# Kernel tuning notes

Hardware: AMD Instinct MI355X
Metric: run time of the kernel (lower is better)

The kernel has to match this reference:

```python
import jax, jax.numpy as jnp
import numpy as np

DIM = 1024
MEM = 512
HEAD = DIM // 2


def setup_inputs() -> dict:
    key = jax.random.key(0)
    k0, k1, k2, k3, k4 = jax.random.split(key, 5)
    x = jax.random.normal(k0, (4, 8192, DIM), dtype=jnp.float32)
    keys_real = jax.random.normal(k1, (MEM, HEAD), dtype=jnp.float32) * 0.02
    keys_imag = jax.random.normal(k2, (MEM, HEAD), dtype=jnp.float32) * 0.02
    values_real = jax.random.normal(k3, (MEM, HEAD), dtype=jnp.float32) * 0.02
    values_imag = jax.random.normal(k4, (MEM, HEAD), dtype=jnp.float32) * 0.02
    return {"x": x, "keys_real": keys_real, "keys_imag": keys_imag,
            "values_real": values_real, "values_imag": values_imag}


def reference(x, keys_real, keys_imag, values_real, values_imag):
    input_shape = x.shape
    temperature = HEAD ** (-0.5)
    x_flat = x.reshape(-1, DIM)                       # [N, dim]
    q, p = jnp.split(x_flat, 2, axis=-1)              # each [N, head]
    # dual real/imag score matmuls summed -> energy [N, mem]
    energy = jnp.einsum('nh,mh->nm', q, keys_real) + jnp.einsum('nh,mh->nm', p, keys_imag)
    attn = jax.nn.softmax(energy * temperature, axis=-1)
    out_real = jnp.einsum('nm,mh->nh', attn, values_real)
    out_imag = jnp.einsum('nm,mh->nh', attn, values_imag)
    return jnp.concatenate([out_real, out_imag], axis=-1).reshape(input_shape)
```

## Files before the change

kernel.cpp:

```cpp
#include <hip/hip_runtime.h>


#define DIMX   1024
#define MEMN   512
#define NROWS  32768
#define TEMP   0.04419417382415922f

typedef __bf16 bf16;
typedef __bf16 bf16x8 __attribute__((ext_vector_type(8)));
typedef float  f32x4  __attribute__((ext_vector_type(4)));

__device__ __forceinline__ void gl_b16x8(bf16x8& d, const bf16* p) {
    asm volatile("global_load_dwordx4 %0, %1, off" : "=v"(d) : "v"(p));
}
__device__ __forceinline__ void gl_f32x4(f32x4& d, const float* p) {
    asm volatile("global_load_dwordx4 %0, %1, off" : "=v"(d) : "v"(p));
}
#define VMW(N)     do { asm volatile("s_waitcnt vmcnt(" #N ")" ::: "memory"); \
                        __builtin_amdgcn_sched_barrier(0); } while (0)
#define WAITBAR(N) do { asm volatile("s_waitcnt vmcnt(" #N ") lgkmcnt(0)\n\t" \
                        "s_barrier" ::: "memory");                            \
                        __builtin_amdgcn_sched_barrier(0); } while (0)

__global__ __launch_bounds__(256) void pack_kv_kernel(const float* __restrict__ kr,
                                                      const float* __restrict__ ki,
                                                      const float* __restrict__ vr,
                                                      const float* __restrict__ vi,
                                                      bf16* __restrict__ Kb,
                                                      bf16* __restrict__ Vb) {
    const int idx = blockIdx.x * 256 + threadIdx.x;
    const int e = idx & 7, l = (idx >> 3) & 63;
    const int lm = l & 15, g = l >> 4;
    {
        const int t = (idx >> 9) & 31, c = idx >> 14;
        const int row = t * 16 + lm, k = c * 32 + g * 8 + e;
        const float v = (k < 512) ? kr[row * 512 + k] : ki[row * 512 + (k - 512)];
        Kb[idx] = (bf16)v;
    }
    {
        const int t = (idx >> 9) & 63, c = idx >> 15;
        const int h = t * 16 + lm, m = c * 32 + g * 8 + e;
        const float v = (h < 512) ? vr[m * 512 + h] : vi[m * 512 + (h - 512)];
        Vb[idx] = (bf16)v;
    }
}

__global__ __launch_bounds__(256, 2) void fused_kernel(
        const float* __restrict__ x,
        const bf16*  __restrict__ Kb,
        const bf16*  __restrict__ Vb,
        float* __restrict__ out) {
    __shared__ __align__(16) char smem[65536];
    float (*red)[4][2] = (float (*)[4][2])(smem + 16384);
    char* Pl = smem;

    const int tid  = threadIdx.x;
    const int wv   = tid >> 6, lane = tid & 63;
    const int lm   = lane & 15, g = lane >> 4;
    const int rowB = blockIdx.x * 64;

    const int sr = tid >> 2, sc = tid & 3;
    const float* xsrc = x + (size_t)(rowB + sr) * DIMX + sc * 16;

    const bf16* kbase = Kb + (wv * 8) * 512 + lane * 8;

    f32x4 acc[4][8] = {};
    f32x4 xa0, xa1, xa2, xa3;
    bf16x8 kfA[8], kfB[8];

#define K_PREF(DST, C) { _Pragma("unroll") for (int j = 0; j < 8; ++j)         \
        gl_b16x8(DST[j], kbase + (size_t)(C) * 16384 + j * 512); }
#define X_PREF(P) { gl_f32x4(xa0, xsrc + (P) * 64);                            \
                    gl_f32x4(xa1, xsrc + (P) * 64 + 4);                        \
                    gl_f32x4(xa2, xsrc + (P) * 64 + 8);                        \
                    gl_f32x4(xa3, xsrc + (P) * 64 + 12); }
#define X_WR(B) { bf16x8 w0, w1;                                               \
    w0[0]=(bf16)xa0[0]; w0[1]=(bf16)xa0[1]; w0[2]=(bf16)xa0[2]; w0[3]=(bf16)xa0[3]; \
    w0[4]=(bf16)xa1[0]; w0[5]=(bf16)xa1[1]; w0[6]=(bf16)xa1[2]; w0[7]=(bf16)xa1[3]; \
    w1[0]=(bf16)xa2[0]; w1[1]=(bf16)xa2[1]; w1[2]=(bf16)xa2[2]; w1[3]=(bf16)xa2[3]; \
    w1[4]=(bf16)xa3[0]; w1[5]=(bf16)xa3[1]; w1[6]=(bf16)xa3[2]; w1[7]=(bf16)xa3[3]; \
    *(bf16x8*)(smem + (B) * 8192 + sr * 128 + (((2 * sc)     ^ (sr & 7)) << 4)) = w0; \
    *(bf16x8*)(smem + (B) * 8192 + sr * 128 + (((2 * sc + 1) ^ (sr & 7)) << 4)) = w1; }
#define COMPUTE_E(PB, S, KF) { bf16x8 af[4];                                   \
    _Pragma("unroll") for (int i = 0; i < 4; ++i) { const int r = i * 16 + lm; \
        af[i] = *(const bf16x8*)(smem + (PB) * 8192 + r * 128                  \
                                 + (((((S) * 4) + g) ^ (r & 7)) << 4)); }      \
    __builtin_amdgcn_s_setprio(1);                                             \
    _Pragma("unroll") for (int i = 0; i < 4; ++i)                              \
        _Pragma("unroll") for (int j = 0; j < 8; ++j)                          \
            acc[i][j] = __builtin_amdgcn_mfma_f32_16x16x32_bf16(               \
                af[i], KF[j], acc[i][j], 0, 0, 0);                             \
    __builtin_amdgcn_s_setprio(0); }

    X_PREF(0);
    K_PREF(kfA, 0);
    VMW(8);
    X_WR(0);
    X_PREF(1);
    WAITBAR(12);

    for (int p = 0; p < 14; ++p) {
        const int pb = p & 1;
        K_PREF(kfB, 2 * p + 1);
        VMW(12);
        COMPUTE_E(pb, 0, kfA);
        K_PREF(kfA, 2 * p + 2);
        VMW(8);
        COMPUTE_E(pb, 1, kfB);
        X_WR(pb ^ 1);
        X_PREF(p + 2);
        WAITBAR(12);
    }
    K_PREF(kfB, 29);
    VMW(12);
    COMPUTE_E(0, 0, kfA);
    K_PREF(kfA, 30);
    VMW(8);
    COMPUTE_E(0, 1, kfB);
    X_WR(1);
    WAITBAR(8);
    K_PREF(kfB, 31);
    VMW(8);
    COMPUTE_E(1, 0, kfA);
    VMW(0);
    COMPUTE_E(1, 1, kfB);

#undef K_PREF
#undef X_PREF
#undef X_WR
#undef COMPUTE_E

    float fac[4][4];
    #pragma unroll
    for (int i = 0; i < 4; ++i) {
        #pragma unroll
        for (int rg = 0; rg < 4; ++rg) {
            float m = acc[i][0][rg] * TEMP;
            #pragma unroll
            for (int j = 1; j < 8; ++j) m = fmaxf(m, acc[i][j][rg] * TEMP);
            m = fmaxf(m, __shfl_xor(m, 1));
            m = fmaxf(m, __shfl_xor(m, 2));
            m = fmaxf(m, __shfl_xor(m, 4));
            m = fmaxf(m, __shfl_xor(m, 8));
            float s = 0.f;
            #pragma unroll
            for (int j = 0; j < 8; ++j) {
                const float v = __expf(acc[i][j][rg] * TEMP - m);
                acc[i][j][rg] = v;
                s += v;
            }
            s += __shfl_xor(s, 1);
            s += __shfl_xor(s, 2);
            s += __shfl_xor(s, 4);
            s += __shfl_xor(s, 8);
            const int rr = i * 16 + g * 4 + rg;
            if (lm == 0) { red[rr][wv][0] = m; red[rr][wv][1] = s; }
            fac[i][rg] = m;
        }
    }
    __syncthreads();
    #pragma unroll
    for (int i = 0; i < 4; ++i) {
        #pragma unroll
        for (int rg = 0; rg < 4; ++rg) {
            const int rr = i * 16 + g * 4 + rg;
            const float m0 = red[rr][0][0], s0 = red[rr][0][1];
            const float m1 = red[rr][1][0], s1 = red[rr][1][1];
            const float m2 = red[rr][2][0], s2 = red[rr][2][1];
            const float m3 = red[rr][3][0], s3 = red[rr][3][1];
            const float M  = fmaxf(fmaxf(m0, m1), fmaxf(m2, m3));
            const float S  = s0 * __expf(m0 - M) + s1 * __expf(m1 - M)
                           + s2 * __expf(m2 - M) + s3 * __expf(m3 - M);
            fac[i][rg] = __expf(fac[i][rg] - M) / S;
        }
    }
    __syncthreads();

    {
        const int cb = wv * 16 + (lm >> 3);
        const int ce = (lm & 7) * 2;
        #pragma unroll
        for (int i = 0; i < 4; ++i) {
            #pragma unroll
            for (int rg = 0; rg < 4; ++rg) {
                const int row = i * 16 + g * 4 + rg;
                const int rx  = row & 7;
                const float f = fac[i][rg];
                char* prow = Pl + row * 1024 + ce;
                #pragma unroll
                for (int j = 0; j < 8; ++j)
                    *(bf16*)(prow + (((cb + j * 2) ^ rx) << 4))
                        = (bf16)(acc[i][j][rg] * f);
            }
        }
    }
    __syncthreads();

#define PV_COMPUTE(BF, KS) { bf16x8 af[4];                                     \
    _Pragma("unroll") for (int i = 0; i < 4; ++i) { const int r = i * 16 + lm; \
        af[i] = *(const bf16x8*)(Pl + r * 1024                                 \
                                 + ((((KS) * 4 + g) ^ (r & 7)) << 4)); }       \
    __builtin_amdgcn_s_setprio(1);                                             \
    _Pragma("unroll") for (int i = 0; i < 4; ++i)                              \
        _Pragma("unroll") for (int j = 0; j < 8; ++j)                          \
            acc[i][j] = __builtin_amdgcn_mfma_f32_16x16x32_bf16(               \
                af[i], BF[j], acc[i][j], 0, 0, 0);                             \
    __builtin_amdgcn_s_setprio(0); }
#define V_PREF(DST, KS) { _Pragma("unroll") for (int j = 0; j < 8; ++j)        \
        gl_b16x8(DST[j], vb + (size_t)(KS) * 32768 + j * 512); }

    #pragma unroll
    for (int h = 0; h < 2; ++h) {
        #pragma unroll
        for (int i = 0; i < 4; ++i)
            #pragma unroll
            for (int j = 0; j < 8; ++j)
                acc[i][j] = (f32x4){0.f, 0.f, 0.f, 0.f};

        const bf16* vb = Vb + (size_t)(wv * 16 + h * 8) * 512 + lane * 8;
        bf16x8 bv0[8], bv1[8];
        V_PREF(bv0, 0);
        for (int ks = 0; ks < 14; ks += 2) {
            V_PREF(bv1, ks + 1); VMW(8); PV_COMPUTE(bv0, ks);
            V_PREF(bv0, ks + 2); VMW(8); PV_COMPUTE(bv1, ks + 1);
        }
        V_PREF(bv1, 15); VMW(8); PV_COMPUTE(bv0, 14);
        VMW(0);          PV_COMPUTE(bv1, 15);

        const int c0 = wv * 256 + h * 128 + lm;
        #pragma unroll
        for (int i = 0; i < 4; ++i) {
            #pragma unroll
            for (int j = 0; j < 8; ++j) {
                #pragma unroll
                for (int rg = 0; rg < 4; ++rg)
                    out[(size_t)(rowB + i * 16 + g * 4 + rg) * DIMX
                        + (c0 + j * 16)] = acc[i][j][rg];
            }
        }
    }

#undef PV_COMPUTE
#undef V_PREF
}

extern "C" void kernel_launch(void* const* d_in, const int* in_sizes, int n_in,
                              void* d_out, int out_size, void* d_ws, size_t ws_size,
                              hipStream_t stream) {
    const float* x  = (const float*)d_in[0];
    const float* kr = (const float*)d_in[1];
    const float* ki = (const float*)d_in[2];
    const float* vr = (const float*)d_in[3];
    const float* vi = (const float*)d_in[4];
    float* out = (float*)d_out;

    char* ws = (char*)d_ws;
    bf16* Kb = (bf16*)ws;
    bf16* Vb = (bf16*)(ws + 1048576);

    pack_kv_kernel<<<2048, 256, 0, stream>>>(kr, ki, vr, vi, Kb, Vb);
    fused_kernel<<<512, 256, 0, stream>>>(x, Kb, Vb, out);
}
```

Measured before the change: 274.0 us.

## Split fused attention block across eight waves with half-width per-wave tiles

Doubles the threads per block from 256 to 512, so each wave covers half as many memory slots in the score stage and half as many output columns in the PV stage. The cross-wave softmax reduction now combines eight partial max/sum pairs instead of four. The aim is more resident waves per CU, to hide load latency and raise MFMA occupancy, with fewer registers per thread. In exchange, each wave re-reads the same A fragments from shared memory and issues more K/V loads per unit of math, and the launch-bound hint of four blocks per CU cannot be met given the 64KB of LDS per block.

```diff
diff --git a/kernel.cpp b/kernel.cpp
--- a/kernel.cpp
+++ b/kernel.cpp
@@ -45,13 +45,13 @@
     }
 }
 
-__global__ __launch_bounds__(256, 2) void fused_kernel(
+__global__ __launch_bounds__(512, 4) void fused_kernel(
         const float* __restrict__ x,
         const bf16*  __restrict__ Kb,
         const bf16*  __restrict__ Vb,
         float* __restrict__ out) {
     __shared__ __align__(16) char smem[65536];
-    float (*red)[4][2] = (float (*)[4][2])(smem + 16384);
+    float (*red)[8][2] = (float (*)[8][2])(smem + 16384);
     char* Pl = smem;
 
     const int tid  = threadIdx.x;
@@ -59,68 +59,63 @@
     const int lm   = lane & 15, g = lane >> 4;
     const int rowB = blockIdx.x * 64;
 
-    const int sr = tid >> 2, sc = tid & 3;
-    const float* xsrc = x + (size_t)(rowB + sr) * DIMX + sc * 16;
-
-    const bf16* kbase = Kb + (wv * 8) * 512 + lane * 8;
-
-    f32x4 acc[4][8] = {};
-    f32x4 xa0, xa1, xa2, xa3;
-    bf16x8 kfA[8], kfB[8];
-
-#define K_PREF(DST, C) { _Pragma("unroll") for (int j = 0; j < 8; ++j)         \
+    const int sr = tid >> 3, sc = tid & 7;
+    const float* xsrc = x + (size_t)(rowB + sr) * DIMX + sc * 8;
+
+    const bf16* kbase = Kb + (wv * 4) * 512 + lane * 8;
+
+    f32x4 acc[4][4] = {};
+    f32x4 xa0, xa1;
+    bf16x8 kfA[4], kfB[4];
+
+#define K_PREF(DST, C) { _Pragma("unroll") for (int j = 0; j < 4; ++j)         \
         gl_b16x8(DST[j], kbase + (size_t)(C) * 16384 + j * 512); }
 #define X_PREF(P) { gl_f32x4(xa0, xsrc + (P) * 64);                            \
-                    gl_f32x4(xa1, xsrc + (P) * 64 + 4);                        \
-                    gl_f32x4(xa2, xsrc + (P) * 64 + 8);                        \
-                    gl_f32x4(xa3, xsrc + (P) * 64 + 12); }
-#define X_WR(B) { bf16x8 w0, w1;                                               \
-    w0[0]=(bf16)xa0[0]; w0[1]=(bf16)xa0[1]; w0[2]=(bf16)xa0[2]; w0[3]=(bf16)xa0[3]; \
-    w0[4]=(bf16)xa1[0]; w0[5]=(bf16)xa1[1]; w0[6]=(bf16)xa1[2]; w0[7]=(bf16)xa1[3]; \
-    w1[0]=(bf16)xa2[0]; w1[1]=(bf16)xa2[1]; w1[2]=(bf16)xa2[2]; w1[3]=(bf16)xa2[3]; \
-    w1[4]=(bf16)xa3[0]; w1[5]=(bf16)xa3[1]; w1[6]=(bf16)xa3[2]; w1[7]=(bf16)xa3[3]; \
-    *(bf16x8*)(smem + (B) * 8192 + sr * 128 + (((2 * sc)     ^ (sr & 7)) << 4)) = w0; \
-    *(bf16x8*)(smem + (B) * 8192 + sr * 128 + (((2 * sc + 1) ^ (sr & 7)) << 4)) = w1; }
+                    gl_f32x4(xa1, xsrc + (P) * 64 + 4); }
+#define X_WR(B) { bf16x8 w;                                                    \
+    w[0]=(bf16)xa0[0]; w[1]=(bf16)xa0[1]; w[2]=(bf16)xa0[2]; w[3]=(bf16)xa0[3]; \
+    w[4]=(bf16)xa1[0]; w[5]=(bf16)xa1[1]; w[6]=(bf16)xa1[2]; w[7]=(bf16)xa1[3]; \
+    *(bf16x8*)(smem + (B) * 8192 + sr * 128 + ((sc ^ (sr & 7)) << 4)) = w; }
 #define COMPUTE_E(PB, S, KF) { bf16x8 af[4];                                   \
     _Pragma("unroll") for (int i = 0; i < 4; ++i) { const int r = i * 16 + lm; \
         af[i] = *(const bf16x8*)(smem + (PB) * 8192 + r * 128                  \
                                  + (((((S) * 4) + g) ^ (r & 7)) << 4)); }      \
     __builtin_amdgcn_s_setprio(1);                                             \
     _Pragma("unroll") for (int i = 0; i < 4; ++i)                              \
-        _Pragma("unroll") for (int j = 0; j < 8; ++j)                          \
+        _Pragma("unroll") for (int j = 0; j < 4; ++j)                          \
             acc[i][j] = __builtin_amdgcn_mfma_f32_16x16x32_bf16(               \
                 af[i], KF[j], acc[i][j], 0, 0, 0);                             \
     __builtin_amdgcn_s_setprio(0); }
 
     X_PREF(0);
     K_PREF(kfA, 0);
-    VMW(8);
+    VMW(4);
     X_WR(0);
     X_PREF(1);
-    WAITBAR(12);
+    WAITBAR(6);
 
     for (int p = 0; p < 14; ++p) {
         const int pb = p & 1;
         K_PREF(kfB, 2 * p + 1);
-        VMW(12);
+        VMW(6);
         COMPUTE_E(pb, 0, kfA);
         K_PREF(kfA, 2 * p + 2);
-        VMW(8);
+        VMW(4);
         COMPUTE_E(pb, 1, kfB);
         X_WR(pb ^ 1);
         X_PREF(p + 2);
-        WAITBAR(12);
+        WAITBAR(6);
     }
     K_PREF(kfB, 29);
-    VMW(12);
+    VMW(6);
     COMPUTE_E(0, 0, kfA);
     K_PREF(kfA, 30);
-    VMW(8);
+    VMW(4);
     COMPUTE_E(0, 1, kfB);
     X_WR(1);
-    WAITBAR(8);
+    WAITBAR(4);
     K_PREF(kfB, 31);
-    VMW(8);
+    VMW(4);
     COMPUTE_E(1, 0, kfA);
     VMW(0);
     COMPUTE_E(1, 1, kfB);
@@ -137,14 +132,14 @@
         for (int rg = 0; rg < 4; ++rg) {
             float m = acc[i][0][rg] * TEMP;
             #pragma unroll
-            for (int j = 1; j < 8; ++j) m = fmaxf(m, acc[i][j][rg] * TEMP);
+            for (int j = 1; j < 4; ++j) m = fmaxf(m, acc[i][j][rg] * TEMP);
             m = fmaxf(m, __shfl_xor(m, 1));
             m = fmaxf(m, __shfl_xor(m, 2));
             m = fmaxf(m, __shfl_xor(m, 4));
             m = fmaxf(m, __shfl_xor(m, 8));
             float s = 0.f;
             #pragma unroll
-            for (int j = 0; j < 8; ++j) {
+            for (int j = 0; j < 4; ++j) {
                 const float v = __expf(acc[i][j][rg] * TEMP - m);
                 acc[i][j][rg] = v;
                 s += v;
@@ -164,20 +159,20 @@
         #pragma unroll
         for (int rg = 0; rg < 4; ++rg) {
             const int rr = i * 16 + g * 4 + rg;
-            const float m0 = red[rr][0][0], s0 = red[rr][0][1];
-            const float m1 = red[rr][1][0], s1 = red[rr][1][1];
-            const float m2 = red[rr][2][0], s2 = red[rr][2][1];
-            const float m3 = red[rr][3][0], s3 = red[rr][3][1];
-            const float M  = fmaxf(fmaxf(m0, m1), fmaxf(m2, m3));
-            const float S  = s0 * __expf(m0 - M) + s1 * __expf(m1 - M)
-                           + s2 * __expf(m2 - M) + s3 * __expf(m3 - M);
+            float M = red[rr][0][0];
+            #pragma unroll
+            for (int w = 1; w < 8; ++w) M = fmaxf(M, red[rr][w][0]);
+            float S = 0.f;
+            #pragma unroll
+            for (int w = 0; w < 8; ++w)
+                S += red[rr][w][1] * __expf(red[rr][w][0] - M);
             fac[i][rg] = __expf(fac[i][rg] - M) / S;
         }
     }
     __syncthreads();
 
     {
-        const int cb = wv * 16 + (lm >> 3);
+        const int cb = wv * 8 + (lm >> 3);
         const int ce = (lm & 7) * 2;
         #pragma unroll
         for (int i = 0; i < 4; ++i) {
@@ -188,7 +183,7 @@
                 const float f = fac[i][rg];
                 char* prow = Pl + row * 1024 + ce;
                 #pragma unroll
-                for (int j = 0; j < 8; ++j)
+                for (int j = 0; j < 4; ++j)
                     *(bf16*)(prow + (((cb + j * 2) ^ rx) << 4))
                         = (bf16)(acc[i][j][rg] * f);
             }
@@ -202,11 +197,11 @@
                                  + ((((KS) * 4 + g) ^ (r & 7)) << 4)); }       \
     __builtin_amdgcn_s_setprio(1);                                             \
     _Pragma("unroll") for (int i = 0; i < 4; ++i)                              \
-        _Pragma("unroll") for (int j = 0; j < 8; ++j)                          \
+        _Pragma("unroll") for (int j = 0; j < 4; ++j)                          \
             acc[i][j] = __builtin_amdgcn_mfma_f32_16x16x32_bf16(               \
                 af[i], BF[j], acc[i][j], 0, 0, 0);                             \
     __builtin_amdgcn_s_setprio(0); }
-#define V_PREF(DST, KS) { _Pragma("unroll") for (int j = 0; j < 8; ++j)        \
+#define V_PREF(DST, KS) { _Pragma("unroll") for (int j = 0; j < 4; ++j)        \
         gl_b16x8(DST[j], vb + (size_t)(KS) * 32768 + j * 512); }
 
     #pragma unroll
@@ -214,24 +209,24 @@
         #pragma unroll
         for (int i = 0; i < 4; ++i)
             #pragma unroll
-            for (int j = 0; j < 8; ++j)
+            for (int j = 0; j < 4; ++j)
                 acc[i][j] = (f32x4){0.f, 0.f, 0.f, 0.f};
 
-        const bf16* vb = Vb + (size_t)(wv * 16 + h * 8) * 512 + lane * 8;
-        bf16x8 bv0[8], bv1[8];
+        const bf16* vb = Vb + (size_t)(wv * 8 + h * 4) * 512 + lane * 8;
+        bf16x8 bv0[4], bv1[4];
         V_PREF(bv0, 0);
         for (int ks = 0; ks < 14; ks += 2) {
-            V_PREF(bv1, ks + 1); VMW(8); PV_COMPUTE(bv0, ks);
-            V_PREF(bv0, ks + 2); VMW(8); PV_COMPUTE(bv1, ks + 1);
-        }
-        V_PREF(bv1, 15); VMW(8); PV_COMPUTE(bv0, 14);
+            V_PREF(bv1, ks + 1); VMW(4); PV_COMPUTE(bv0, ks);
+            V_PREF(bv0, ks + 2); VMW(4); PV_COMPUTE(bv1, ks + 1);
+        }
+        V_PREF(bv1, 15); VMW(4); PV_COMPUTE(bv0, 14);
         VMW(0);          PV_COMPUTE(bv1, 15);
 
-        const int c0 = wv * 256 + h * 128 + lm;
+        const int c0 = wv * 128 + h * 64 + lm;
         #pragma unroll
         for (int i = 0; i < 4; ++i) {
             #pragma unroll
-            for (int j = 0; j < 8; ++j) {
+            for (int j = 0; j < 4; ++j) {
                 #pragma unroll
                 for (int rg = 0; rg < 4; ++rg)
                     out[(size_t)(rowB + i * 16 + g * 4 + rg) * DIMX
@@ -259,5 +254,5 @@
     bf16* Vb = (bf16*)(ws + 1048576);
 
     pack_kv_kernel<<<2048, 256, 0, stream>>>(kr, ki, vr, vi, Kb, Vb);
-    fused_kernel<<<512, 256, 0, stream>>>(x, Kb, Vb, out);
-}
+    fused_kernel<<<512, 512, 0, stream>>>(x, Kb, Vb, out);
+}
```

Result: slower. 286.5 us (+4.5%).
